# Kernel optimization log

Hardware: AMD Instinct MI355X
Metric: run time of the kernel (lower is better)

Reference implementation:

```python
import math
import jax, jax.numpy as jnp
import numpy as np

NUM_HEADS = 12
ALPHA, BETA, GAMMA = 1.9, 3.8, 15.2  # get_rpe_config(ratio=1.9)
SKIP = 1


def _rp_bucket(side):
    """iRPE euclidean contextual bucket table for a side x side grid + 1 cls token."""
    beta_int = int(BETA)
    coords = np.stack(np.meshgrid(np.arange(side), np.arange(side), indexing='ij'), -1).reshape(-1, 2)
    diff = coords[:, None, :] - coords[None, :, :]
    dis = np.round(np.sqrt((diff ** 2).sum(-1).astype(np.float64)))  # rounded euclidean distance
    far = np.clip(np.round(ALPHA + np.log(np.maximum(dis, 1e-9) / ALPHA) / math.log(GAMMA / ALPHA) * (BETA - ALPHA)), None, BETA)
    idx = np.where(dis <= ALPHA, dis, far).astype(np.int32) + beta_int
    num_buckets = 2 * beta_int + 1  # 7
    L = side * side
    full = np.full((L + SKIP, L + SKIP), num_buckets, dtype=np.int32)  # extra bucket for cls
    full[SKIP:, SKIP:] = idx
    return full, num_buckets + 1  # table [P,P], total buckets = 8


def setup_inputs() -> dict:
    key = jax.random.key(0)
    ks = jax.random.split(key, 8)
    B, P, n_mod, C = 64, 197, 2, 768
    N = 1 + (P - 1) * n_mod  # 393
    hd = C // NUM_HEADS
    rp_bucket, n_buckets = _rp_bucket(int(math.sqrt(P - SKIP)))
    s = 0.02
    return {
        'x': jax.random.normal(ks[0], (B, N, C), jnp.float32),
        'q_learned': jax.random.normal(ks[1], (1, 1, C), jnp.float32) * s,
        'pos_embed': jax.random.normal(ks[2], (1, P, C), jnp.float32) * s,
        'wk': jax.random.normal(ks[3], (C, C), jnp.float32) * s,
        'wv': jax.random.normal(ks[4], (C, C), jnp.float32) * s,
        'rpe_w': jax.random.normal(ks[5], (hd, n_buckets), jnp.float32) * s,  # shared_head ctx lookup table
        'proj_w': jax.random.normal(ks[6], (C, C), jnp.float32) * s,
        'proj_b': jnp.zeros((C,), jnp.float32),
        'rp_bucket': jnp.asarray(rp_bucket),  # [P, P] int32
    }


def reference(x, q_learned, pos_embed, wk, wv, rpe_w, proj_w, proj_b, rp_bucket):
    B, N, C = x.shape
    H = NUM_HEADS
    hd = C // H
    P = rp_bucket.shape[0]
    n_mod = (N - 1) // (P - 1)
    scale = hd ** -0.5

    q_ = jnp.broadcast_to(q_learned + pos_embed, (B, P, C))
    q = q_.reshape(B, P, H, hd).transpose(0, 2, 1, 3)                    # bhpd
    k = (x @ wk.T).reshape(B, N, H, hd).transpose(0, 2, 1, 3)            # bhnd
    v = (x @ wv.T).reshape(B, N, H, hd).transpose(0, 2, 1, 3)            # bhnd

    attn = jnp.einsum('bhpd,bhnd->bhpn', q, k) * scale                   # [B,H,P,N]

    # contextual RPE on keys: lookup = q @ table, gathered by rp_bucket[i, j]
    lookup = jnp.einsum('bhpd,du->bhpu', q, rpe_w)                        # [B,H,P,n_buckets]
    bias = lookup[:, :, jnp.arange(P)[:, None], rp_bucket]                # [B,H,P,P]
    bias = jnp.concatenate([bias[..., :1], jnp.tile(bias[..., 1:], (1, 1, 1, n_mod))], axis=-1)
    attn = jax.nn.softmax(attn + bias, axis=-1)

    out = jnp.einsum('bhpn,bhnd->bhpd', attn, v).transpose(0, 2, 1, 3).reshape(B, P, C)
    return out @ proj_w.T + proj_b
```

## Files before the change

### kernel.cpp

```cpp
#include <hip/hip_runtime.h>

typedef unsigned short u16;
typedef short bf16x8 __attribute__((ext_vector_type(8)));
typedef float f32x4 __attribute__((ext_vector_type(4)));
typedef const __attribute__((address_space(1))) void* gptr_t;
typedef __attribute__((address_space(3))) void* lptr_t;

#define B_   64
#define N_   393
#define C_   768
#define H_   12
#define HD_  64
#define P_   197
#define BIAS_N 416
#define PPAD 208
#define VTP  448
#define M_KV (B_ * N_)
#define M_PR (B_ * P_)
#define SCALE_L2E 0.180336879f
#define PPITCH 70

__device__ __forceinline__ u16 f2bf(float f) {
    unsigned u = __float_as_uint(f);
    return (u16)((u + 0x7FFFu + ((u >> 16) & 1u)) >> 16);
}
__device__ __forceinline__ unsigned cvt_pk_bf16(float lo, float hi) {
    unsigned r;
    asm("v_cvt_pk_bf16_f32 %0, %1, %2" : "=v"(r) : "v"(lo), "v"(hi));
    return r;
}
__device__ __forceinline__ float exp2_fast(float x) {
    float r;
    asm("v_exp_f32 %0, %1" : "=v"(r) : "v"(x));
    return r;
}

__global__ __launch_bounds__(256) void conv_prep1(
    const float* __restrict__ x, const float* __restrict__ wk,
    const float* __restrict__ wv, const float* __restrict__ pw,
    const float* __restrict__ q_learned, const float* __restrict__ pos_embed,
    const float* __restrict__ rpe_w,
    u16* __restrict__ xh, u16* __restrict__ wkvh, u16* __restrict__ pwh,
    u16* __restrict__ qh, float* __restrict__ lk)
{
    __shared__ float q_s[C_];
    const int bx = blockIdx.x, t = threadIdx.x;
    if (bx < 20592) {
        const int XN4 = 19316736 / 4;
        const int WN4 = 589824 / 4;
        int i = bx * 256 + t;
        const float* src; u16* dst; int off;
        if (i < XN4) { src = x; dst = xh; off = i; }
        else {
            int j = i - XN4;
            int sec = j / WN4;
            off = j - sec * WN4;
            src = sec == 0 ? wk : (sec == 1 ? wv : pw);
            dst = sec == 0 ? wkvh : (sec == 1 ? wkvh + 589824 : pwh);
        }
        float4 v = ((const float4*)src)[off];
        u16 o[4] = {f2bf(v.x), f2bf(v.y), f2bf(v.z), f2bf(v.w)};
        *(uint2*)(dst + off * 4) = *(uint2*)o;
    } else {
        const int p = bx - 20592;
        for (int c = t; c < C_; c += 256) {
            float v = q_learned[c] + pos_embed[p * C_ + c];
            q_s[c] = v;
            qh[p * C_ + c] = f2bf(v);
        }
        __syncthreads();
        if (t < H_ * 8) {
            int h = t >> 3, u = t & 7;
            float s = 0.f;
            #pragma unroll 8
            for (int d = 0; d < HD_; ++d)
                s = fmaf(q_s[h * HD_ + d], rpe_w[d * 8 + u], s);
            lk[(h * P_ + p) * 8 + u] = s;
        }
    }
}

template <bool F32OUT>
__global__ __launch_bounds__(256) void gemm_bf16(
    const u16* __restrict__ A, const u16* __restrict__ Bw,
    u16* __restrict__ Cb, float* __restrict__ Cf, const float* __restrict__ bias,
    int M, int ldc)
{
    __shared__ __align__(16) u16 As[128 * 64];
    __shared__ __align__(16) u16 Bs[128 * 64];

    const int gx = gridDim.x;
    const int nwg = gx * gridDim.y;
    const int orig = blockIdx.y * gx + blockIdx.x;
    const int xcd = orig & 7, rank = orig >> 3;
    const int q = nwg >> 3, r = nwg & 7;
    const int wgid = (xcd < r ? xcd * (q + 1) : r * (q + 1) + (xcd - r) * q) + rank;
    const int n0 = (wgid % gx) * 128;
    const int m0 = (wgid / gx) * 128;

    const int t = threadIdx.x;
    const int w = t >> 6, l = t & 63;
    const int wr = w >> 1, wc = w & 1;
    const int l15 = l & 15, lg = l >> 4;
    const int lrow = l >> 3, lslot = l & 7;
    const int Mc = M - 1;

    f32x4 acc[4][4];
    #pragma unroll
    for (int i = 0; i < 4; ++i)
        #pragma unroll
        for (int j = 0; j < 4; ++j) acc[i][j] = (f32x4){0.f, 0.f, 0.f, 0.f};

    for (int ks = 0; ks < 12; ++ks) {
        const int k0 = ks * 64;
        if (ks) __syncthreads();
        #pragma unroll
        for (int i = 0; i < 4; ++i) {
            const int rbase = w * 32 + i * 8;
            int arow = m0 + rbase + lrow; if (arow > Mc) arow = Mc;
            const int brow = n0 + rbase + lrow;
            const u16* ga = A  + (size_t)arow * 768 + k0 + lslot * 8;
            const u16* gb = Bw + (size_t)brow * 768 + k0 + lslot * 8;
            __builtin_amdgcn_global_load_lds((gptr_t)(const void*)ga,
                                             (lptr_t)(void*)(As + rbase * 64), 16, 0, 0);
            __builtin_amdgcn_global_load_lds((gptr_t)(const void*)gb,
                                             (lptr_t)(void*)(Bs + rbase * 64), 16, 0, 0);
        }
        __syncthreads();
        #pragma unroll
        for (int kk = 0; kk < 2; ++kk) {
            bf16x8 af[4], bfr[4];
            #pragma unroll
            for (int mf = 0; mf < 4; ++mf) {
                af[mf]  = *(const bf16x8*)(As + (wr * 64 + mf * 16 + l15) * 64 + (kk * 4 + lg) * 8);
                bfr[mf] = *(const bf16x8*)(Bs + (wc * 64 + mf * 16 + l15) * 64 + (kk * 4 + lg) * 8);
            }
            #pragma unroll
            for (int mf = 0; mf < 4; ++mf)
                #pragma unroll
                for (int nf = 0; nf < 4; ++nf)
                    acc[mf][nf] = __builtin_amdgcn_mfma_f32_16x16x32_bf16(
                        af[mf], bfr[nf], acc[mf][nf], 0, 0, 0);
        }
    }

    #pragma unroll
    for (int mf = 0; mf < 4; ++mf) {
        #pragma unroll
        for (int nf = 0; nf < 4; ++nf) {
            int col = n0 + wc * 64 + nf * 16 + l15;
            float bb = 0.f;
            if (F32OUT) bb = bias[col];
            #pragma unroll
            for (int rr = 0; rr < 4; ++rr) {
                int m = m0 + wr * 64 + mf * 16 + lg * 4 + rr;
                if (m < M) {
                    if (F32OUT) Cf[(size_t)m * ldc + col] = acc[mf][nf][rr] + bb;
                    else        Cb[(size_t)m * ldc + col] = f2bf(acc[mf][nf][rr]);
                }
            }
        }
    }
}

__global__ __launch_bounds__(256) void vtrans_prep2(
    const u16* __restrict__ KV, u16* __restrict__ Vt,
    const float* __restrict__ lk, const int* __restrict__ rp_bucket,
    float* __restrict__ biasT2)
{
    __shared__ __align__(16) u16 vts[64][68];
    const int bx = blockIdx.x, t = threadIdx.x;
    if (bx < B_ * H_) {
        const int b = bx / H_, h = bx % H_;
        const u16* src = KV + (size_t)b * N_ * 1536 + 768 + h * HD_;
        u16* dst = Vt + (size_t)bx * HD_ * VTP;
        for (int jt = 0; jt < 7; ++jt) {
            const int j0 = jt * 64;
            if (jt) __syncthreads();
            #pragma unroll
            for (int ps = 0; ps < 2; ++ps) {
                int jr = ps * 32 + (t >> 3);
                int dd = (t & 7) * 8;
                int j = j0 + jr;
                bf16x8 v = (bf16x8){0, 0, 0, 0, 0, 0, 0, 0};
                if (j < N_) v = *(const bf16x8*)(src + (size_t)j * 1536 + dd);
                *(bf16x8*)(&vts[jr][dd]) = v;
            }
            __syncthreads();
            #pragma unroll
            for (int ps = 0; ps < 2; ++ps) {
                int idx = t + 256 * ps;
                int d = idx >> 3, ch = idx & 7;
                u16 v[8];
                #pragma unroll
                for (int k = 0; k < 8; ++k) v[k] = vts[ch * 8 + k][d];
                *(bf16x8*)(dst + (size_t)d * VTP + j0 + ch * 8) = *(bf16x8*)v;
            }
        }
    } else {
        const int i = bx - B_ * H_;
        const int h = i / PPAD, p = i % PPAD;
        for (int j = t; j < BIAS_N; j += 256) {
            float v = 0.f;
            if (p < P_ && j < N_) {
                int jm;
                if (j == 0) jm = 0;
                else { jm = j - 1; if (jm >= 196) jm -= 196; jm += 1; }
                int bucket = rp_bucket[p * P_ + jm];
                v = lk[(h * P_ + p) * 8 + bucket] * 1.44269504f;
            }
            biasT2[((size_t)h * PPAD + p) * BIAS_N + j] = v;
        }
    }
}

__global__ __launch_bounds__(256, 4) void attn_flash(
    const u16* __restrict__ qh, const u16* __restrict__ KV,
    const u16* __restrict__ Vt, const float* __restrict__ biasT2,
    u16* __restrict__ Obuf)
{
    __shared__ __align__(16) u16 kk[2][64 * 64];
    __shared__ __align__(16) u16 vv[64 * 64];
    __shared__ __align__(16) u16 pp[64 * PPITCH];

    const int id = blockIdx.x;
    const int work = (id & 7) * 384 + (id >> 3);
    const int ptile = work & 3;
    const int rest = work >> 2;
    const int h = rest % 12;
    const int b = rest / 12;
    const int p0 = ptile * 64;

    const int t = threadIdx.x, w = t >> 6, l = t & 63;
    const int l15 = l & 15, lg = l >> 4;
    const int p0w = p0 + w * 16;
    const int rowp = w * 16 + l15;

    int srow[2], sslot[2], swoff[2];
    #pragma unroll
    for (int i = 0; i < 2; ++i) {
        int c = t + 256 * i;
        srow[i] = c >> 3; sslot[i] = c & 7;
        swoff[i] = srow[i] * 64 + ((sslot[i] ^ (srow[i] & 7)) << 3);
    }

    int prow = p0w + l15; if (prow > P_ - 1) prow = P_ - 1;
    const u16* qp = qh + (size_t)prow * C_ + h * HD_ + lg * 8;
    bf16x8 qf0 = *(const bf16x8*)(qp);
    bf16x8 qf1 = *(const bf16x8*)(qp + 32);

    const u16* Kbase = KV + (size_t)b * (N_ * 1536) + h * HD_;
    const u16* Vbase = Vt + (size_t)(b * H_ + h) * (HD_ * VTP);
    const int pcl = (p0 + rowp) > (PPAD - 1) ? (PPAD - 1) : (p0 + rowp);
    const float* bias_row = biasT2 + ((size_t)h * PPAD + pcl) * BIAS_N;

    bf16x8 raK[2], raV[2];
    #pragma unroll
    for (int i = 0; i < 2; ++i)
        raK[i] = *(const bf16x8*)(Kbase + (size_t)srow[i] * 1536 + sslot[i] * 8);
    #pragma unroll
    for (int i = 0; i < 2; ++i) *(bf16x8*)(&kk[0][swoff[i]]) = raK[i];
    #pragma unroll
    for (int i = 0; i < 2; ++i)
        raV[i] = *(const bf16x8*)(Vbase + (size_t)srow[i] * VTP + sslot[i] * 8);
    __syncthreads();

    float s_acc = 0.f;
    f32x4 o[4];
    #pragma unroll
    for (int i = 0; i < 4; ++i) o[i] = (f32x4){0.f, 0.f, 0.f, 0.f};

    #pragma unroll
    for (int nt = 0; nt < 7; ++nt) {
        const u16* kcur = kk[nt & 1];

        f32x4 accs[4];
        #pragma unroll
        for (int i = 0; i < 4; ++i) accs[i] = (f32x4){0.f, 0.f, 0.f, 0.f};
        __builtin_amdgcn_s_setprio(1);
        #pragma unroll
        for (int kc = 0; kc < 2; ++kc)
            #pragma unroll
            for (int sub = 0; sub < 4; ++sub) {
                int row = sub * 16 + l15;
                bf16x8 kb = *(const bf16x8*)(kcur + row * 64 + (((kc * 4 + lg) ^ (row & 7)) << 3));
                accs[sub] = __builtin_amdgcn_mfma_f32_16x16x32_bf16(
                    kb, kc ? qf1 : qf0, accs[sub], 0, 0, 0);
            }
        __builtin_amdgcn_s_setprio(0);

        #pragma unroll
        for (int i = 0; i < 2; ++i) *(bf16x8*)(&vv[swoff[i]]) = raV[i];
        if (nt < 6) {
            #pragma unroll
            for (int i = 0; i < 2; ++i) {
                int rn = (nt + 1) * 64 + srow[i]; if (rn > N_ - 1) rn = N_ - 1;
                raK[i] = *(const bf16x8*)(Kbase + (size_t)rn * 1536 + sslot[i] * 8);
            }
        }

        #pragma unroll
        for (int sub = 0; sub < 4; ++sub) {
            int jb = nt * 64 + sub * 16 + lg * 4;
            float4 b4 = *(const float4*)(bias_row + jb);
            float bb[4] = {b4.x, b4.y, b4.z, b4.w};
            float e[4];
            #pragma unroll
            for (int rr = 0; rr < 4; ++rr) {
                float ev = exp2_fast(fmaf(accs[sub][rr], SCALE_L2E, bb[rr]));
                e[rr] = (jb + rr < N_) ? ev : 0.f;
                s_acc += e[rr];
            }
            unsigned pk01 = cvt_pk_bf16(e[0], e[1]);
            unsigned pk23 = cvt_pk_bf16(e[2], e[3]);
            *(unsigned*)(&pp[rowp * PPITCH + sub * 16 + lg * 4]) = pk01;
            *(unsigned*)(&pp[rowp * PPITCH + sub * 16 + lg * 4 + 2]) = pk23;
        }
        __syncthreads();

        const int kcmax = (nt == 6) ? 1 : 2;
        __builtin_amdgcn_s_setprio(1);
        #pragma unroll
        for (int kc = 0; kc < kcmax; ++kc) {
            bf16x8 pa = *(const bf16x8*)(&pp[rowp * PPITCH + kc * 32 + lg * 8]);
            #pragma unroll
            for (int dsub = 0; dsub < 4; ++dsub) {
                int row = dsub * 16 + l15;
                bf16x8 vb = *(const bf16x8*)(vv + row * 64 + (((kc * 4 + lg) ^ (row & 7)) << 3));
                o[dsub] = __builtin_amdgcn_mfma_f32_16x16x32_bf16(vb, pa, o[dsub], 0, 0, 0);
            }
        }
        __builtin_amdgcn_s_setprio(0);

        if (nt < 6) {
            #pragma unroll
            for (int i = 0; i < 2; ++i) *(bf16x8*)(&kk[(nt + 1) & 1][swoff[i]]) = raK[i];
            #pragma unroll
            for (int i = 0; i < 2; ++i)
                raV[i] = *(const bf16x8*)(Vbase + (size_t)srow[i] * VTP + (nt + 1) * 64 + sslot[i] * 8);
        }
        __syncthreads();
    }

    s_acc += __shfl_xor(s_acc, 16);
    s_acc += __shfl_xor(s_acc, 32);
    float rinv = 1.0f / s_acc;

    int p = p0 + rowp;
    if (p < P_) {
        #pragma unroll
        for (int dsub = 0; dsub < 4; ++dsub) {
            u16 v4[4];
            #pragma unroll
            for (int rr = 0; rr < 4; ++rr) v4[rr] = f2bf(o[dsub][rr] * rinv);
            *(uint2*)(Obuf + ((size_t)b * P_ + p) * C_ + h * HD_ + dsub * 16 + lg * 4) =
                *(uint2*)v4;
        }
    }
}

extern "C" void kernel_launch(void* const* d_in, const int* in_sizes, int n_in,
                              void* d_out, int out_size, void* d_ws, size_t ws_size,
                              hipStream_t stream)
{
    const float* x         = (const float*)d_in[0];
    const float* q_learned = (const float*)d_in[1];
    const float* pos_embed = (const float*)d_in[2];
    const float* wk        = (const float*)d_in[3];
    const float* wv        = (const float*)d_in[4];
    const float* rpe_w     = (const float*)d_in[5];
    const float* proj_w    = (const float*)d_in[6];
    const float* proj_b    = (const float*)d_in[7];
    const int*   rp_bucket = (const int*)d_in[8];
    float* out = (float*)d_out;

    char* ws = (char*)d_ws;
    u16*   xh    = (u16*)(ws);
    u16*   wkvh  = (u16*)(ws + 38633472);
    u16*   pwh   = (u16*)(ws + 40992768);
    u16*   qh    = (u16*)(ws + 42172416);
    float* lk    = (float*)(ws + 42475008);
    float* biasT2= (float*)(ws + 42550784);
    u16*   KV    = (u16*)(ws + 46704128);
    u16*   Vt    = (u16*)(ws + 123971072);
    u16*   Obuf  = (u16*)(ws + 168011264);

    conv_prep1<<<20789, 256, 0, stream>>>(x, wk, wv, proj_w,
                                          q_learned, pos_embed, rpe_w,
                                          xh, wkvh, pwh, qh, lk);

    dim3 gkv(1536 / 128, (M_KV + 127) / 128);
    gemm_bf16<false><<<gkv, 256, 0, stream>>>(xh, wkvh, KV, nullptr, nullptr, M_KV, 1536);

    vtrans_prep2<<<3264, 256, 0, stream>>>(KV, Vt, lk, rp_bucket, biasT2);

    attn_flash<<<3072, 256, 0, stream>>>(qh, KV, Vt, biasT2, Obuf);

    dim3 gpr(768 / 128, (M_PR + 127) / 128);
    gemm_bf16<true><<<gpr, 256, 0, stream>>>(Obuf, pwh, nullptr, out, proj_b, M_PR, 768);
}
```

Measured before the change: 214.7 us.

## Double-buffer V and P tiles in attention to drop one barrier per iteration

The attention kernel now keeps double-buffered LDS tiles for V and the probability matrix P, and prefetches K two tiles ahead. This removes the second __syncthreads in each key-tile iteration. It also skips the dead QK MFMA and exp work on the last partial tile, zero-filling the unused P slots instead. The extra LDS lowers launch bounds from 4 to 3 blocks per CU, trading occupancy for fewer barriers and better overlap.

```diff
diff --git a/kernel.cpp b/kernel.cpp
--- a/kernel.cpp
+++ b/kernel.cpp
@@ -214,14 +214,14 @@
     }
 }
 
-__global__ __launch_bounds__(256, 4) void attn_flash(
+__global__ __launch_bounds__(256, 3) void attn_flash(
     const u16* __restrict__ qh, const u16* __restrict__ KV,
     const u16* __restrict__ Vt, const float* __restrict__ biasT2,
     u16* __restrict__ Obuf)
 {
     __shared__ __align__(16) u16 kk[2][64 * 64];
-    __shared__ __align__(16) u16 vv[64 * 64];
-    __shared__ __align__(16) u16 pp[64 * PPITCH];
+    __shared__ __align__(16) u16 vv[2][64 * 64];
+    __shared__ __align__(16) u16 pp[2][64 * PPITCH];
 
     const int id = blockIdx.x;
     const int work = (id & 7) * 384 + (id >> 3);
@@ -261,6 +261,11 @@
     #pragma unroll
     for (int i = 0; i < 2; ++i) *(bf16x8*)(&kk[0][swoff[i]]) = raK[i];
     #pragma unroll
+    for (int i = 0; i < 2; ++i) {
+        int rn = 64 + srow[i]; if (rn > N_ - 1) rn = N_ - 1;
+        raK[i] = *(const bf16x8*)(Kbase + (size_t)rn * 1536 + sslot[i] * 8);
+    }
+    #pragma unroll
     for (int i = 0; i < 2; ++i)
         raV[i] = *(const bf16x8*)(Vbase + (size_t)srow[i] * VTP + sslot[i] * 8);
     __syncthreads();
@@ -272,7 +277,9 @@
 
     #pragma unroll
     for (int nt = 0; nt < 7; ++nt) {
-        const u16* kcur = kk[nt & 1];
+        const int cur = nt & 1, nxt = cur ^ 1;
+        const u16* kcur = kk[cur];
+        const int submax = (nt == 6) ? 1 : 4;
 
         f32x4 accs[4];
         #pragma unroll
@@ -282,6 +289,7 @@
         for (int kc = 0; kc < 2; ++kc)
             #pragma unroll
             for (int sub = 0; sub < 4; ++sub) {
+                if (sub >= submax) continue;
                 int row = sub * 16 + l15;
                 bf16x8 kb = *(const bf16x8*)(kcur + row * 64 + (((kc * 4 + lg) ^ (row & 7)) << 3));
                 accs[sub] = __builtin_amdgcn_mfma_f32_16x16x32_bf16(
@@ -290,17 +298,27 @@
         __builtin_amdgcn_s_setprio(0);
 
         #pragma unroll
-        for (int i = 0; i < 2; ++i) *(bf16x8*)(&vv[swoff[i]]) = raV[i];
+        for (int i = 0; i < 2; ++i) *(bf16x8*)(&vv[cur][swoff[i]]) = raV[i];
         if (nt < 6) {
             #pragma unroll
+            for (int i = 0; i < 2; ++i) *(bf16x8*)(&kk[nxt][swoff[i]]) = raK[i];
+        }
+        if (nt < 5) {
+            #pragma unroll
             for (int i = 0; i < 2; ++i) {
-                int rn = (nt + 1) * 64 + srow[i]; if (rn > N_ - 1) rn = N_ - 1;
+                int rn = (nt + 2) * 64 + srow[i]; if (rn > N_ - 1) rn = N_ - 1;
                 raK[i] = *(const bf16x8*)(Kbase + (size_t)rn * 1536 + sslot[i] * 8);
             }
         }
+        if (nt < 6) {
+            #pragma unroll
+            for (int i = 0; i < 2; ++i)
+                raV[i] = *(const bf16x8*)(Vbase + (size_t)srow[i] * VTP + (nt + 1) * 64 + sslot[i] * 8);
+        }
 
         #pragma unroll
         for (int sub = 0; sub < 4; ++sub) {
+            if (sub >= submax) continue;
             int jb = nt * 64 + sub * 16 + lg * 4;
             float4 b4 = *(const float4*)(bias_row + jb);
             float bb[4] = {b4.x, b4.y, b4.z, b4.w};
@@ -313,33 +331,29 @@
             }
             unsigned pk01 = cvt_pk_bf16(e[0], e[1]);
             unsigned pk23 = cvt_pk_bf16(e[2], e[3]);
-            *(unsigned*)(&pp[rowp * PPITCH + sub * 16 + lg * 4]) = pk01;
-            *(unsigned*)(&pp[rowp * PPITCH + sub * 16 + lg * 4 + 2]) = pk23;
+            *(unsigned*)(&pp[cur][rowp * PPITCH + sub * 16 + lg * 4]) = pk01;
+            *(unsigned*)(&pp[cur][rowp * PPITCH + sub * 16 + lg * 4 + 2]) = pk23;
+        }
+        if (nt == 6) {
+            *(unsigned*)(&pp[cur][rowp * PPITCH + 16 + lg * 4]) = 0;
+            *(unsigned*)(&pp[cur][rowp * PPITCH + 16 + lg * 4 + 2]) = 0;
         }
         __syncthreads();
 
         const int kcmax = (nt == 6) ? 1 : 2;
         __builtin_amdgcn_s_setprio(1);
         #pragma unroll
-        for (int kc = 0; kc < kcmax; ++kc) {
-            bf16x8 pa = *(const bf16x8*)(&pp[rowp * PPITCH + kc * 32 + lg * 8]);
+        for (int kc = 0; kc < 2; ++kc) {
+            if (kc >= kcmax) continue;
+            bf16x8 pa = *(const bf16x8*)(&pp[cur][rowp * PPITCH + kc * 32 + lg * 8]);
             #pragma unroll
             for (int dsub = 0; dsub < 4; ++dsub) {
                 int row = dsub * 16 + l15;
-                bf16x8 vb = *(const bf16x8*)(vv + row * 64 + (((kc * 4 + lg) ^ (row & 7)) << 3));
+                bf16x8 vb = *(const bf16x8*)(&vv[cur][row * 64 + (((kc * 4 + lg) ^ (row & 7)) << 3)]);
                 o[dsub] = __builtin_amdgcn_mfma_f32_16x16x32_bf16(vb, pa, o[dsub], 0, 0, 0);
             }
         }
         __builtin_amdgcn_s_setprio(0);
-
-        if (nt < 6) {
-            #pragma unroll
-            for (int i = 0; i < 2; ++i) *(bf16x8*)(&kk[(nt + 1) & 1][swoff[i]]) = raK[i];
-            #pragma unroll
-            for (int i = 0; i < 2; ++i)
-                raV[i] = *(const bf16x8*)(Vbase + (size_t)srow[i] * VTP + (nt + 1) * 64 + sslot[i] * 8);
-        }
-        __syncthreads();
     }
 
     s_acc += __shfl_xor(s_acc, 16);
```

Result: no change. 214.9 us, median of 2 (+0.1%).
